# Optimization experiments

Hardware: AMD Instinct MI355X
Metric: run time of the kernel (lower is better)

Reference implementation:

```python
import jax, jax.numpy as jnp
import numpy as np

H = 16  # num_heads (matches init_kwargs)
MASK_VAL = -10000.0


def setup_inputs() -> dict:
    key = jax.random.key(0)
    k1, k2, k3, k4, k5 = jax.random.split(key, 5)
    B, N, C = 2, 2048, 1024
    hidden_states = jax.random.normal(k1, (B, N, C), dtype=jnp.float32)
    encoder_hidden_states = jax.random.normal(k2, (B, N, C), dtype=jnp.float32)
    pad_mask = jax.random.bernoulli(k3, 0.1, (B, N))
    # Linear weights stored as (in, out); scaled ~Xavier so softmax isn't saturated
    W_q = jax.random.normal(k4, (C, C), dtype=jnp.float32) * (C ** -0.5)
    W_c = jax.random.normal(k5, (C, 2 * C), dtype=jnp.float32) * (C ** -0.5)
    return {"hidden_states": hidden_states,
            "encoder_hidden_states": encoder_hidden_states,
            "pad_mask": pad_mask,
            "W_q": W_q,
            "W_c": W_c}


def _split_heads(x, B, N, C):
    # (B, N, C) -> (B, H, N, D)
    return x.reshape(B, N, H, C // H).transpose(0, 2, 1, 3)


def reference(hidden_states, encoder_hidden_states, pad_mask, W_q, W_c):
    B, N, C = hidden_states.shape
    D = C // H
    scaler = D ** -0.5

    q = hidden_states @ W_q                       # (B, N, C)
    kv = encoder_hidden_states @ W_c              # (B, N, 2C)
    k, v = kv[..., :C], kv[..., C:]

    q = _split_heads(q, B, N, C)                  # (B, H, N, D)
    k = _split_heads(k, B, N, C)
    v = _split_heads(v, B, N, C)

    scores = jnp.einsum('bhid,bhjd->bhij', q, k) * scaler  # (B, H, N, N)

    # construct_mask: expanded[b,i,j] = pad_mask[b,i] OR pad_mask[b,j]
    expanded = pad_mask[:, None, :, None] | pad_mask[:, None, None, :]
    scores = jnp.where(expanded, MASK_VAL, scores)

    # max-subtract + softmax (dropout_rate=0 so dropout is identity)
    scores = scores - jax.lax.stop_gradient(scores.max(axis=-1, keepdims=True))
    att_weights = jax.nn.softmax(scores, axis=-1)

    att = jnp.einsum('bhij,bhjd->bhid', att_weights, v)   # (B, H, N, D)
    att = att.transpose(0, 2, 1, 3).reshape(B, N, C)
    return att, att_weights
```

## Files before the change

### kernel.cpp

```cpp
#include <hip/hip_runtime.h>
#include <math.h>

#define B_ 2
#define N_ 2048
#define C_ 1024
#define H_ 16
#define D_ 64

typedef __attribute__((ext_vector_type(8))) short short8v;
typedef __attribute__((ext_vector_type(4))) short short4v;
typedef __attribute__((ext_vector_type(4))) float f32x4;

static __device__ __forceinline__ short f2bf(float f) {
    union { float f; unsigned u; } v; v.f = f;
    unsigned r = v.u + 0x7FFFu + ((v.u >> 16) & 1u);
    return (short)(r >> 16);
}

static __device__ __forceinline__ void splitbf(float f, short& h, short& l) {
    union { float f; unsigned u; } v; v.f = f;
    const unsigned uh = v.u & 0xFFFF0000u;
    h = (short)(uh >> 16);
    union { unsigned u; float f; } w; w.u = uh;
    union { float f; unsigned u; } x; x.f = f - w.f;
    l = (short)(x.u >> 16);
}

#define GKSTR 40

__global__ __launch_bounds__(256) void gemm_x3(const float* __restrict__ A,
                                               const float* __restrict__ Bm,
                                               short* __restrict__ Cm,
                                               int K, int N) {
    __shared__ __align__(16) short Ahi[128][GKSTR];
    __shared__ __align__(16) short Alo[128][GKSTR];
    __shared__ __align__(16) short Bhi[64][GKSTR];
    __shared__ __align__(16) short Blo[64][GKSTR];

    const int t  = threadIdx.x;
    const int w  = t >> 6;
    const int l  = t & 63;
    const int lq = l & 15;
    const int hq = l >> 4;
    const int wr = w >> 1;
    const int wc = w & 1;
    const int m0 = blockIdx.y * 128;
    const int n0 = blockIdx.x * 64;

    const int arow = t >> 3;
    const int akc  = (t & 7) * 4;
    const int bn   = t & 63;
    const int bkq  = w * 8;

    f32x4 acc[4][2];
#pragma unroll
    for (int mi = 0; mi < 4; ++mi)
#pragma unroll
        for (int ni = 0; ni < 2; ++ni) acc[mi][ni] = (f32x4){0.f, 0.f, 0.f, 0.f};

    float4 af[4];
    float  bf[8];
#pragma unroll
    for (int it = 0; it < 4; ++it)
        af[it] = *(const float4*)&A[(size_t)(m0 + arow + it * 32) * K + akc];
#pragma unroll
    for (int kk = 0; kk < 8; ++kk)
        bf[kk] = Bm[(size_t)(bkq + kk) * N + n0 + bn];

    short4v ah[4], al[4];
    short8v bh, bl;
#pragma unroll
    for (int it = 0; it < 4; ++it) {
        short h, lo2;
        splitbf(af[it].x, h, lo2); ah[it][0] = h; al[it][0] = lo2;
        splitbf(af[it].y, h, lo2); ah[it][1] = h; al[it][1] = lo2;
        splitbf(af[it].z, h, lo2); ah[it][2] = h; al[it][2] = lo2;
        splitbf(af[it].w, h, lo2); ah[it][3] = h; al[it][3] = lo2;
    }
#pragma unroll
    for (int kk = 0; kk < 8; ++kk) {
        short h, lo2;
        splitbf(bf[kk], h, lo2); bh[kk] = h; bl[kk] = lo2;
    }

    for (int k0 = 0; k0 < K; k0 += 32) {
        __syncthreads();
#pragma unroll
        for (int it = 0; it < 4; ++it) {
            *(short4v*)&Ahi[arow + it * 32][akc] = ah[it];
            *(short4v*)&Alo[arow + it * 32][akc] = al[it];
        }
        *(short8v*)&Bhi[bn][bkq] = bh;
        *(short8v*)&Blo[bn][bkq] = bl;
        __syncthreads();

        const int kn = k0 + 32;
        if (kn < K) {
#pragma unroll
            for (int it = 0; it < 4; ++it)
                af[it] = *(const float4*)&A[(size_t)(m0 + arow + it * 32) * K + kn + akc];
#pragma unroll
            for (int kk = 0; kk < 8; ++kk)
                bf[kk] = Bm[(size_t)(kn + bkq + kk) * N + n0 + bn];
        }

        short8v amh[4], aml[4], bnh[2], bnl[2];
#pragma unroll
        for (int mi = 0; mi < 4; ++mi) {
            amh[mi] = *(const short8v*)&Ahi[wr * 64 + mi * 16 + lq][hq * 8];
            aml[mi] = *(const short8v*)&Alo[wr * 64 + mi * 16 + lq][hq * 8];
        }
#pragma unroll
        for (int ni = 0; ni < 2; ++ni) {
            bnh[ni] = *(const short8v*)&Bhi[wc * 32 + ni * 16 + lq][hq * 8];
            bnl[ni] = *(const short8v*)&Blo[wc * 32 + ni * 16 + lq][hq * 8];
        }
#pragma unroll
        for (int mi = 0; mi < 4; ++mi)
#pragma unroll
            for (int ni = 0; ni < 2; ++ni) {
                acc[mi][ni] = __builtin_amdgcn_mfma_f32_16x16x32_bf16(amh[mi], bnh[ni], acc[mi][ni], 0, 0, 0);
                acc[mi][ni] = __builtin_amdgcn_mfma_f32_16x16x32_bf16(amh[mi], bnl[ni], acc[mi][ni], 0, 0, 0);
                acc[mi][ni] = __builtin_amdgcn_mfma_f32_16x16x32_bf16(aml[mi], bnh[ni], acc[mi][ni], 0, 0, 0);
            }

        if (kn < K) {
#pragma unroll
            for (int it = 0; it < 4; ++it) {
                short h, lo2;
                splitbf(af[it].x, h, lo2); ah[it][0] = h; al[it][0] = lo2;
                splitbf(af[it].y, h, lo2); ah[it][1] = h; al[it][1] = lo2;
                splitbf(af[it].z, h, lo2); ah[it][2] = h; al[it][2] = lo2;
                splitbf(af[it].w, h, lo2); ah[it][3] = h; al[it][3] = lo2;
            }
#pragma unroll
            for (int kk = 0; kk < 8; ++kk) {
                short h, lo2;
                splitbf(bf[kk], h, lo2); bh[kk] = h; bl[kk] = lo2;
            }
        }
    }

#pragma unroll
    for (int mi = 0; mi < 4; ++mi)
#pragma unroll
        for (int ni = 0; ni < 2; ++ni) {
            const int col = n0 + wc * 32 + ni * 16 + lq;
#pragma unroll
            for (int r = 0; r < 4; ++r) {
                const int row = m0 + wr * 64 + mi * 16 + hq * 4 + r;
                Cm[(size_t)row * N + col] = f2bf(acc[mi][ni][r]);
            }
        }
}

__global__ __launch_bounds__(256) void v_transpose(const short* __restrict__ kv_bf,
                                                   short* __restrict__ vt) {
    __shared__ __align__(16) short Ls[128][72];
    const int t  = threadIdx.x;
    const int jt = blockIdx.x * 128;
    const int h  = blockIdx.y;
    const int b  = blockIdx.z;
    const short* src = kv_bf + (size_t)b * N_ * 2 * C_ + C_ + h * D_;
#pragma unroll
    for (int it = 0; it < 4; ++it) {
        const int idx = it * 256 + t;
        const int j = idx >> 3, d0 = (idx & 7) * 8;
        *(short8v*)&Ls[j][d0] = *(const short8v*)&src[(size_t)(jt + j) * (2 * C_) + d0];
    }
    __syncthreads();
    short* dst = vt + ((size_t)(b * H_ + h)) * D_ * N_;
#pragma unroll
    for (int it = 0; it < 4; ++it) {
        const int idx = it * 256 + t;
        const int d  = idx >> 4;
        const int j0 = (idx & 15) * 8;
        short8v s;
#pragma unroll
        for (int jj = 0; jj < 8; ++jj) s[jj] = Ls[j0 + jj][d];
        *(short8v*)&dst[(size_t)d * N_ + jt + j0] = s;
    }
}

#define KSTR 72
#define VSTR 136
#define PSTR 136

__global__ __launch_bounds__(256) void attn_mfma(const short* __restrict__ q,
                                                 const short* __restrict__ kv,
                                                 const short* __restrict__ vtg,
                                                 const int* __restrict__ mask,
                                                 float* __restrict__ out_att,
                                                 float* __restrict__ out_w) {
    __shared__ __align__(16) short Ks[128][KSTR];
    __shared__ __align__(16) short Vt[64][VSTR];
    __shared__ __align__(16) short Ps[4][16][PSTR];
    __shared__ float linv_s[4][16];
    __shared__ int   mcol_s[128];

    const int t  = threadIdx.x;
    const int w  = t >> 6;
    const int l  = t & 63;
    const int lq = l & 15;
    const int hq = l >> 4;

    const int lin = blockIdx.x;
    const int swz = (lin & 7) * 128 + (lin >> 3);
    const int qb = swz & 31;
    const int h  = (swz >> 5) & 15;
    const int b  = swz >> 9;
    const int i0 = qb * 64 + w * 16;

    const int sj = t >> 3;
    const int sd = (t & 7) * 8;
    const int vd = t >> 4;
    const int vj = (t & 15) * 8;

    short8v qa[2];
    {
        const short* qrow = q + ((size_t)(b * N_ + i0 + lq)) * C_ + h * D_;
        qa[0] = *(const short8v*)&qrow[hq * 8];
        qa[1] = *(const short8v*)&qrow[32 + hq * 8];
    }

    int mr[4];
#pragma unroll
    for (int r = 0; r < 4; ++r) mr[r] = mask[b * N_ + i0 + hq * 4 + r];

    const short* kbase = kv + (size_t)b * N_ * 2 * C_ + h * D_;
    const short* vtb   = vtg + ((size_t)(b * H_ + h)) * D_ * N_;

    float lsum[4] = {0.f, 0.f, 0.f, 0.f};
    short8v kr[4];
    int mpre = 0;
#pragma unroll
    for (int it = 0; it < 4; ++it)
        kr[it] = *(const short8v*)&kbase[(size_t)(it * 32 + sj) * (2 * C_) + sd];
    if (t < 128) mpre = mask[b * N_ + t];

    for (int tile = 0; tile < 16; ++tile) {
        __syncthreads();
#pragma unroll
        for (int it = 0; it < 4; ++it)
            *(short8v*)&Ks[it * 32 + sj][sd] = kr[it];
        if (t < 128) mcol_s[t] = mpre;
        __syncthreads();

        if (tile < 15) {
            const int jn = (tile + 1) * 128;
#pragma unroll
            for (int it = 0; it < 4; ++it)
                kr[it] = *(const short8v*)&kbase[(size_t)(jn + it * 32 + sj) * (2 * C_) + sd];
            if (t < 128) mpre = mask[b * N_ + jn + t];
        }

#pragma unroll
        for (int cb = 0; cb < 8; ++cb) {
            f32x4 acc = {0.f, 0.f, 0.f, 0.f};
            const short8v b0 = *(short8v*)&Ks[cb * 16 + lq][hq * 8];
            const short8v b1 = *(short8v*)&Ks[cb * 16 + lq][32 + hq * 8];
            acc = __builtin_amdgcn_mfma_f32_16x16x32_bf16(qa[0], b0, acc, 0, 0, 0);
            acc = __builtin_amdgcn_mfma_f32_16x16x32_bf16(qa[1], b1, acc, 0, 0, 0);
            const int mc = mcol_s[cb * 16 + lq];
#pragma unroll
            for (int r = 0; r < 4; ++r)
                lsum[r] += mr[r] ? 1.0f : (mc ? 0.0f : __expf(acc[r] * 0.125f));
        }
    }
    float inv[4];
#pragma unroll
    for (int r = 0; r < 4; ++r) {
        float s = lsum[r];
#pragma unroll
        for (int off = 1; off < 16; off <<= 1) s += __shfl_xor(s, off, 64);
        inv[r] = 1.0f / s;
    }
    if (lq == 0)
#pragma unroll
        for (int r = 0; r < 4; ++r) linv_s[w][hq * 4 + r] = inv[r];

    float* wrow[4];
#pragma unroll
    for (int r = 0; r < 4; ++r)
        wrow[r] = out_w + ((size_t)((b * H_ + h) * N_ + i0 + hq * 4 + r)) * N_;

    f32x4 oacc[4];
#pragma unroll
    for (int db = 0; db < 4; ++db) oacc[db] = (f32x4){0.f, 0.f, 0.f, 0.f};

    short8v vr[4];
#pragma unroll
    for (int it = 0; it < 4; ++it) {
        kr[it] = *(const short8v*)&kbase[(size_t)(it * 32 + sj) * (2 * C_) + sd];
        vr[it] = *(const short8v*)&vtb[(size_t)(it * 16 + vd) * N_ + vj];
    }
    if (t < 128) mpre = mask[b * N_ + t];

    for (int tile = 0; tile < 16; ++tile) {
        const int jt = tile * 128;
        __syncthreads();
#pragma unroll
        for (int it = 0; it < 4; ++it) {
            *(short8v*)&Ks[it * 32 + sj][sd] = kr[it];
            *(short8v*)&Vt[it * 16 + vd][vj] = vr[it];
        }
        if (t < 128) mcol_s[t] = mpre;
        __syncthreads();

        if (tile < 15) {
            const int jn = jt + 128;
#pragma unroll
            for (int it = 0; it < 4; ++it) {
                kr[it] = *(const short8v*)&kbase[(size_t)(jn + it * 32 + sj) * (2 * C_) + sd];
                vr[it] = *(const short8v*)&vtb[(size_t)(it * 16 + vd) * N_ + jn + vj];
            }
            if (t < 128) mpre = mask[b * N_ + jn + t];
        }

#pragma unroll
        for (int cb = 0; cb < 8; ++cb) {
            f32x4 acc = {0.f, 0.f, 0.f, 0.f};
            const short8v b0 = *(short8v*)&Ks[cb * 16 + lq][hq * 8];
            const short8v b1 = *(short8v*)&Ks[cb * 16 + lq][32 + hq * 8];
            acc = __builtin_amdgcn_mfma_f32_16x16x32_bf16(qa[0], b0, acc, 0, 0, 0);
            acc = __builtin_amdgcn_mfma_f32_16x16x32_bf16(qa[1], b1, acc, 0, 0, 0);
            const int mc   = mcol_s[cb * 16 + lq];
            const int jcol = cb * 16 + lq;
#pragma unroll
            for (int r = 0; r < 4; ++r) {
                const float ev = mr[r] ? 1.0f : (mc ? 0.0f : __expf(acc[r] * 0.125f));
                wrow[r][jt + jcol] = ev * inv[r];
                Ps[w][hq * 4 + r][jcol] = f2bf(ev);
            }
        }
        __syncthreads();

#pragma unroll
        for (int db = 0; db < 4; ++db)
#pragma unroll
            for (int kb = 0; kb < 4; ++kb) {
                const short8v va = *(short8v*)&Vt[db * 16 + lq][kb * 32 + hq * 8];
                const short8v pb = *(short8v*)&Ps[w][lq][kb * 32 + hq * 8];
                oacc[db] = __builtin_amdgcn_mfma_f32_16x16x32_bf16(va, pb, oacc[db], 0, 0, 0);
            }
    }

    {
        const float invi = linv_s[w][lq];
        const size_t abase = ((size_t)(b * N_ + i0 + lq)) * C_ + h * D_;
#pragma unroll
        for (int db = 0; db < 4; ++db)
#pragma unroll
            for (int r = 0; r < 4; ++r)
                out_att[abase + db * 16 + hq * 4 + r] = oacc[db][r] * invi;
    }
}

extern "C" void kernel_launch(void* const* d_in, const int* in_sizes, int n_in,
                              void* d_out, int out_size, void* d_ws, size_t ws_size,
                              hipStream_t stream) {
    const float* hs   = (const float*)d_in[0];
    const float* ehs  = (const float*)d_in[1];
    const int*   mask = (const int*)d_in[2];
    const float* W_q  = (const float*)d_in[3];
    const float* W_c  = (const float*)d_in[4];

    float* out_att = (float*)d_out;
    float* out_w   = (float*)d_out + (size_t)B_ * N_ * C_;

    short* qbf  = (short*)d_ws;
    short* kvbf = qbf + (size_t)B_ * N_ * C_;
    short* vt   = kvbf + (size_t)B_ * N_ * 2 * C_;

    gemm_x3<<<dim3(C_ / 64, (B_ * N_) / 128), 256, 0, stream>>>(
        hs, W_q, qbf, C_, C_);
    gemm_x3<<<dim3((2 * C_) / 64, (B_ * N_) / 128), 256, 0, stream>>>(
        ehs, W_c, kvbf, C_, 2 * C_);
    v_transpose<<<dim3(N_ / 128, H_, B_), 256, 0, stream>>>(kvbf, vt);

    attn_mfma<<<dim3(1024), 256, 0, stream>>>(
        qbf, kvbf, vt, mask, out_att, out_w);
}
```

Measured before the change: 323.5 us.

## Process 32 query rows per wave to reuse K/V tiles across two row groups

Each wave now handles two 16-row query groups instead of one, so a block covers 128 query rows and the grid halves to 512 blocks. Each K and V tile loaded into shared memory serves twice as many MFMA operations, which cuts global K/V traffic and the number of barrier rounds per unit of work. The cost is more registers (two Q fragments, doubled accumulators), a larger Ps buffer, and fewer blocks, which may reduce occupancy and latency hiding on the GPU's compute units. The kernel is likely dominated by writing the fp32 attention-weight matrix, so the gain may be limited.

New measurement: 321.5 us. About the same (-0.6%).

```diff
diff --git a/kernel.cpp b/kernel.cpp
--- a/kernel.cpp
+++ b/kernel.cpp
@@ -194,8 +194,8 @@
                                                  float* __restrict__ out_w) {
     __shared__ __align__(16) short Ks[128][KSTR];
     __shared__ __align__(16) short Vt[64][VSTR];
-    __shared__ __align__(16) short Ps[4][16][PSTR];
-    __shared__ float linv_s[4][16];
+    __shared__ __align__(16) short Ps[4][32][PSTR];
+    __shared__ float linv_s[4][32];
     __shared__ int   mcol_s[128];
 
     const int t  = threadIdx.x;
@@ -205,32 +205,40 @@
     const int hq = l >> 4;
 
     const int lin = blockIdx.x;
-    const int swz = (lin & 7) * 128 + (lin >> 3);
-    const int qb = swz & 31;
-    const int h  = (swz >> 5) & 15;
-    const int b  = swz >> 9;
-    const int i0 = qb * 64 + w * 16;
+    const int swz = (lin & 7) * 64 + (lin >> 3);
+    const int qb = swz & 15;
+    const int h  = (swz >> 4) & 15;
+    const int b  = swz >> 8;
+    const int i0 = qb * 128 + w * 32;
 
     const int sj = t >> 3;
     const int sd = (t & 7) * 8;
     const int vd = t >> 4;
     const int vj = (t & 15) * 8;
 
-    short8v qa[2];
-    {
-        const short* qrow = q + ((size_t)(b * N_ + i0 + lq)) * C_ + h * D_;
-        qa[0] = *(const short8v*)&qrow[hq * 8];
-        qa[1] = *(const short8v*)&qrow[32 + hq * 8];
-    }
-
-    int mr[4];
-#pragma unroll
-    for (int r = 0; r < 4; ++r) mr[r] = mask[b * N_ + i0 + hq * 4 + r];
+    short8v qa[2][2];
+#pragma unroll
+    for (int g = 0; g < 2; ++g) {
+        const short* qrow = q + ((size_t)(b * N_ + i0 + g * 16 + lq)) * C_ + h * D_;
+        qa[g][0] = *(const short8v*)&qrow[hq * 8];
+        qa[g][1] = *(const short8v*)&qrow[32 + hq * 8];
+    }
+
+    int mr[2][4];
+#pragma unroll
+    for (int g = 0; g < 2; ++g)
+#pragma unroll
+        for (int r = 0; r < 4; ++r) mr[g][r] = mask[b * N_ + i0 + g * 16 + hq * 4 + r];
 
     const short* kbase = kv + (size_t)b * N_ * 2 * C_ + h * D_;
     const short* vtb   = vtg + ((size_t)(b * H_ + h)) * D_ * N_;
 
-    float lsum[4] = {0.f, 0.f, 0.f, 0.f};
+    float lsum[2][4];
+#pragma unroll
+    for (int g = 0; g < 2; ++g)
+#pragma unroll
+        for (int r = 0; r < 4; ++r) lsum[g][r] = 0.f;
+
     short8v kr[4];
     int mpre = 0;
 #pragma unroll
@@ -256,37 +264,46 @@
 
 #pragma unroll
         for (int cb = 0; cb < 8; ++cb) {
-            f32x4 acc = {0.f, 0.f, 0.f, 0.f};
             const short8v b0 = *(short8v*)&Ks[cb * 16 + lq][hq * 8];
             const short8v b1 = *(short8v*)&Ks[cb * 16 + lq][32 + hq * 8];
-            acc = __builtin_amdgcn_mfma_f32_16x16x32_bf16(qa[0], b0, acc, 0, 0, 0);
-            acc = __builtin_amdgcn_mfma_f32_16x16x32_bf16(qa[1], b1, acc, 0, 0, 0);
             const int mc = mcol_s[cb * 16 + lq];
 #pragma unroll
-            for (int r = 0; r < 4; ++r)
-                lsum[r] += mr[r] ? 1.0f : (mc ? 0.0f : __expf(acc[r] * 0.125f));
-        }
-    }
-    float inv[4];
-#pragma unroll
-    for (int r = 0; r < 4; ++r) {
-        float s = lsum[r];
-#pragma unroll
-        for (int off = 1; off < 16; off <<= 1) s += __shfl_xor(s, off, 64);
-        inv[r] = 1.0f / s;
-    }
+            for (int g = 0; g < 2; ++g) {
+                f32x4 acc = {0.f, 0.f, 0.f, 0.f};
+                acc = __builtin_amdgcn_mfma_f32_16x16x32_bf16(qa[g][0], b0, acc, 0, 0, 0);
+                acc = __builtin_amdgcn_mfma_f32_16x16x32_bf16(qa[g][1], b1, acc, 0, 0, 0);
+#pragma unroll
+                for (int r = 0; r < 4; ++r)
+                    lsum[g][r] += mr[g][r] ? 1.0f : (mc ? 0.0f : __expf(acc[r] * 0.125f));
+            }
+        }
+    }
+    float inv[2][4];
+#pragma unroll
+    for (int g = 0; g < 2; ++g)
+#pragma unroll
+        for (int r = 0; r < 4; ++r) {
+            float s = lsum[g][r];
+#pragma unroll
+            for (int off = 1; off < 16; off <<= 1) s += __shfl_xor(s, off, 64);
+            inv[g][r] = 1.0f / s;
+        }
     if (lq == 0)
 #pragma unroll
-        for (int r = 0; r < 4; ++r) linv_s[w][hq * 4 + r] = inv[r];
-
-    float* wrow[4];
-#pragma unroll
-    for (int r = 0; r < 4; ++r)
-        wrow[r] = out_w + ((size_t)((b * H_ + h) * N_ + i0 + hq * 4 + r)) * N_;
-
-    f32x4 oacc[4];
-#pragma unroll
-    for (int db = 0; db < 4; ++db) oacc[db] = (f32x4){0.f, 0.f, 0.f, 0.f};
+        for (int g = 0; g < 2; ++g)
+#pragma unroll
+            for (int r = 0; r < 4; ++r) linv_s[w][g * 16 + hq * 4 + r] = inv[g][r];
+
+    float* wbase[2];
+#pragma unroll
+    for (int g = 0; g < 2; ++g)
+        wbase[g] = out_w + ((size_t)((b * H_ + h) * N_ + i0 + g * 16 + hq * 4)) * N_;
+
+    f32x4 oacc[4][2];
+#pragma unroll
+    for (int db = 0; db < 4; ++db)
+#pragma unroll
+        for (int g = 0; g < 2; ++g) oacc[db][g] = (f32x4){0.f, 0.f, 0.f, 0.f};
 
     short8v vr[4];
 #pragma unroll
@@ -319,40 +336,50 @@
 
 #pragma unroll
         for (int cb = 0; cb < 8; ++cb) {
-            f32x4 acc = {0.f, 0.f, 0.f, 0.f};
             const short8v b0 = *(short8v*)&Ks[cb * 16 + lq][hq * 8];
             const short8v b1 = *(short8v*)&Ks[cb * 16 + lq][32 + hq * 8];
-            acc = __builtin_amdgcn_mfma_f32_16x16x32_bf16(qa[0], b0, acc, 0, 0, 0);
-            acc = __builtin_amdgcn_mfma_f32_16x16x32_bf16(qa[1], b1, acc, 0, 0, 0);
             const int mc   = mcol_s[cb * 16 + lq];
             const int jcol = cb * 16 + lq;
 #pragma unroll
-            for (int r = 0; r < 4; ++r) {
-                const float ev = mr[r] ? 1.0f : (mc ? 0.0f : __expf(acc[r] * 0.125f));
-                wrow[r][jt + jcol] = ev * inv[r];
-                Ps[w][hq * 4 + r][jcol] = f2bf(ev);
-            }
-        }
-        __syncthreads();
-
+            for (int g = 0; g < 2; ++g) {
+                f32x4 acc = {0.f, 0.f, 0.f, 0.f};
+                acc = __builtin_amdgcn_mfma_f32_16x16x32_bf16(qa[g][0], b0, acc, 0, 0, 0);
+                acc = __builtin_amdgcn_mfma_f32_16x16x32_bf16(qa[g][1], b1, acc, 0, 0, 0);
+#pragma unroll
+                for (int r = 0; r < 4; ++r) {
+                    const float ev = mr[g][r] ? 1.0f : (mc ? 0.0f : __expf(acc[r] * 0.125f));
+                    wbase[g][(size_t)r * N_ + jt + jcol] = ev * inv[g][r];
+                    Ps[w][g * 16 + hq * 4 + r][jcol] = f2bf(ev);
+                }
+            }
+        }
+        __syncthreads();
+
+        short8v pb[2][4];
+#pragma unroll
+        for (int kb = 0; kb < 4; ++kb) {
+            pb[0][kb] = *(short8v*)&Ps[w][lq][kb * 32 + hq * 8];
+            pb[1][kb] = *(short8v*)&Ps[w][16 + lq][kb * 32 + hq * 8];
+        }
 #pragma unroll
         for (int db = 0; db < 4; ++db)
 #pragma unroll
             for (int kb = 0; kb < 4; ++kb) {
                 const short8v va = *(short8v*)&Vt[db * 16 + lq][kb * 32 + hq * 8];
-                const short8v pb = *(short8v*)&Ps[w][lq][kb * 32 + hq * 8];
-                oacc[db] = __builtin_amdgcn_mfma_f32_16x16x32_bf16(va, pb, oacc[db], 0, 0, 0);
-            }
-    }
-
-    {
-        const float invi = linv_s[w][lq];
-        const size_t abase = ((size_t)(b * N_ + i0 + lq)) * C_ + h * D_;
+                oacc[db][0] = __builtin_amdgcn_mfma_f32_16x16x32_bf16(va, pb[0][kb], oacc[db][0], 0, 0, 0);
+                oacc[db][1] = __builtin_amdgcn_mfma_f32_16x16x32_bf16(va, pb[1][kb], oacc[db][1], 0, 0, 0);
+            }
+    }
+
+#pragma unroll
+    for (int g = 0; g < 2; ++g) {
+        const float invi = linv_s[w][g * 16 + lq];
+        const size_t abase = ((size_t)(b * N_ + i0 + g * 16 + lq)) * C_ + h * D_;
 #pragma unroll
         for (int db = 0; db < 4; ++db)
 #pragma unroll
             for (int r = 0; r < 4; ++r)
-                out_att[abase + db * 16 + hq * 4 + r] = oacc[db][r] * invi;
+                out_att[abase + db * 16 + hq * 4 + r] = oacc[db][g][r] * invi;
     }
 }
 
@@ -378,6 +405,6 @@
         ehs, W_c, kvbf, C_, 2 * C_);
     v_transpose<<<dim3(N_ / 128, H_, B_), 256, 0, stream>>>(kvbf, vt);
 
-    attn_mfma<<<dim3(1024), 256, 0, stream>>>(
+    attn_mfma<<<dim3(512), 256, 0, stream>>>(
         qbf, kvbf, vt, mask, out_att, out_w);
 }
```
